# Kernel optimization log

Measured on AMD Instinct MI355X. Metric: run time of the kernel, lower is better.

## Reference

```python
import jax, jax.numpy as jnp
import numpy as np

T_STEPS = 64      # AR order p
MAX_T = 65536     # trajectory length
BATCH = 256       # number of sampled trajectories
STD = 0.3


def setup_inputs() -> dict:
    key = jax.random.key(0)
    k1, k2, k3 = jax.random.split(key, 3)
    raw = jax.random.normal(k1, (T_STEPS,), dtype=jnp.float32)
    # torch init: params / sum(|params|)
    params = raw / jnp.sum(jnp.abs(raw))
    bias = jax.random.uniform(k2, (1,), dtype=jnp.float32)
    noise = jax.random.normal(k3, (BATCH, MAX_T), dtype=jnp.float32)
    return {"params": params, "bias": bias, "noise": noise}


def _ar_means(params, bias, length):
    """AR(p) recurrence: mean_i = sum_k params[k] * x[i-1-k] + bias, x init = 0.
    State holds the last p values, most-recent-first (matches the reversed
    indexing inputs[i-1 : i-p-1 : -1] in the torch code)."""
    p = params.shape[0]

    def step(state, _):
        new = jnp.dot(state, params) + bias[0]
        state = jnp.concatenate([new[None], state[:-1]])
        return state, new

    init = jnp.zeros((p,), dtype=params.dtype)
    _, means = jax.lax.scan(step, init, None, length=length)
    return means  # [length]


def reference(params, bias, noise):
    # means of the Normal over the trajectory (deterministic, shared by batch)
    means = _ar_means(params, bias, noise.shape[1])  # [T]
    # reparameterized sample: actions = mean + std * eps, eps ~ N(0, 1)
    actions = means[None, :] + jnp.asarray(STD, noise.dtype) * noise  # [B, T]
    return actions
```

## Files before the change

### kernel.cpp

```cpp
#include <hip/hip_runtime.h>

#define T_LEN   65536
#define P       64
#define BASE    4096
#define K1_THREADS 256
#define W_TILE  1024
#define BCHUNK  8
#define VOFF    65536

typedef float f4 __attribute__((ext_vector_type(4)));


__constant__ unsigned char  TL_DST[14] = {2, 3,4, 6,5,8, 7,10,12,9, 14,11,13, 15};
__constant__ unsigned char  TL_SRC[14] = {1, 2,2, 3,4,4, 6,5,6,8, 7,10,12, 14};
__constant__ unsigned char  TL_DBL[14] = {1, 0,1, 1,0,1, 0,1,1,0, 1,0,0, 0};
__constant__ unsigned short TL_W[14]   = {192, 256,128, 192,256,64, 256,192,128,256, 192,256,256, 256};
__constant__ unsigned char  TL_OFF[7]  = {0,1,3,6,10,13,14};

__device__ __forceinline__ void tapV_wave(const float* __restrict__ td, int wd,
                                          const float* __restrict__ p,
                                          float* __restrict__ Vdst, int lane) {
    const int j = lane;
    float w0 = 0.f, w1 = 0.f, w2 = 0.f, w3 = 0.f;
    #pragma unroll
    for (int mm = 0; mm < 16; ++mm) w0 = fmaf(p[mm + j],      td[wd - 1  - mm], w0);
    #pragma unroll
    for (int mm = 0; mm < 16; ++mm) w1 = fmaf(p[16 + mm + j], td[wd - 17 - mm], w1);
    #pragma unroll
    for (int mm = 0; mm < 16; ++mm) w2 = fmaf(p[32 + mm + j], td[wd - 33 - mm], w2);
    #pragma unroll
    for (int mm = 0; mm < 16; ++mm) w3 = fmaf(p[48 + mm + j], td[wd - 49 - mm], w3);
    const float wj  = ((w0 + w1) + w2) + w3;
    const float wm1 = __shfl_up(wj, 1);
    Vdst[j] = (j == 0) ? wj : (wj - wm1);
    if (j == 63) Vdst[64] = 0.0f - wj;
}

__global__ __launch_bounds__(K1_THREADS, 1) void ar_k1(const float* __restrict__ params,
                                                       float* __restrict__ R) {
    __shared__ __align__(16) float Rl[BASE];
    __shared__ float p[128];
    __shared__ __align__(16) float Vs[68];
    __shared__ __align__(16) float Vnode[16][68];
    __shared__ __align__(16) float Tn[8][256];
    __shared__ __align__(16) float Tw[4][256];
    const int tid = threadIdx.x;
    if (tid < 128) p[tid] = (tid < P) ? params[tid] : 0.f;
    __syncthreads();

    if (tid < 64) {
        float z = 0.f;
        const float pk = p[tid];
        #pragma unroll 1
        for (int t = 0; t < 64; ++t) {
            float y  = __shfl(z, 0) + 1.0f;
            float zn = __shfl_down(z, 1);
            if (tid == 63) zn = 0.f;
            z = fmaf(pk, y, zn);
            if (tid == 0) Rl[t] = y;
        }
    }
    __syncthreads();

    #pragma unroll 1
    for (int L = 64; L <= BASE / 2; L <<= 1) {
        if (tid < 64) tapV_wave(Rl, L, p, Vs, tid);
        __syncthreads();
        if (tid < P) {
            const int tau = tid;
            float acc = Rl[tau];
            #pragma unroll
            for (int i = 0; i < P; ++i) {
                const int idx = (tau - i) > 0 ? (tau - i) : 0;
                const float v = (i <= tau) ? Vs[i] : 0.f;
                acc = fmaf(v, Rl[idx], acc);
            }
            Rl[L + tau] = acc;
        }
        {
            const f4* __restrict__ Rl4 = reinterpret_cast<const f4*>(Rl);
            f4* __restrict__ Rl4w = reinterpret_cast<f4*>(Rl);
            const f4* __restrict__ V4 = reinterpret_cast<const f4*>(Vs);
            const int nq = (L - 64) >> 2;
            #pragma unroll 1
            for (int q = tid; q < nq; q += K1_THREADS) {
                f4 w4[17];
                #pragma unroll
                for (int j = 0; j < 17; ++j) w4[j] = Rl4[q + j];
                float a0 = w4[16].x, a1 = w4[16].y, a2 = w4[16].z, a3 = w4[16].w;
                #pragma unroll
                for (int g = 0; g < 16; ++g) {
                    const f4 v  = V4[g];
                    const f4 hi = w4[16 - g];
                    const f4 lo = w4[15 - g];
                    a0 = fmaf(v.x, hi.x, a0); a1 = fmaf(v.x, hi.y, a1);
                    a2 = fmaf(v.x, hi.z, a2); a3 = fmaf(v.x, hi.w, a3);
                    a0 = fmaf(v.y, lo.w, a0); a1 = fmaf(v.y, hi.x, a1);
                    a2 = fmaf(v.y, hi.y, a2); a3 = fmaf(v.y, hi.z, a3);
                    a0 = fmaf(v.z, lo.z, a0); a1 = fmaf(v.z, lo.w, a1);
                    a2 = fmaf(v.z, hi.x, a2); a3 = fmaf(v.z, hi.y, a3);
                    a0 = fmaf(v.w, lo.y, a0); a1 = fmaf(v.w, lo.z, a1);
                    a2 = fmaf(v.w, lo.w, a2); a3 = fmaf(v.w, hi.x, a3);
                }
                const float v64 = Vs[64];
                a0 = fmaf(v64, w4[0].x, a0); a1 = fmaf(v64, w4[0].y, a1);
                a2 = fmaf(v64, w4[0].z, a2); a3 = fmaf(v64, w4[0].w, a3);
                f4 o; o.x = a0; o.y = a1; o.z = a2; o.w = a3;
                Rl4w[((L + 64) >> 2) + q] = o;
            }
        }
        __syncthreads();
    }

    #pragma unroll 1
    for (int j4 = tid; j4 < BASE / 4; j4 += K1_THREADS)
        reinterpret_cast<f4*>(R)[j4] = reinterpret_cast<const f4*>(Rl)[j4];

    if (tid < 64) tapV_wave(Rl + 3840, 256, p, Vnode[1], tid);
    __syncthreads();

    #pragma unroll 1
    for (int lvl = 0; lvl < 6; ++lvl) {
        const int w = tid >> 6, lane = tid & 63;
        const int n0 = TL_OFF[lvl], n1 = TL_OFF[lvl + 1];
        const int e = n0 + w;
        float* td = nullptr;
        int wd = 0;
        if (e < n1) {
            const int dst = TL_DST[e], src = TL_SRC[e];
            wd = TL_W[e];
            const float* __restrict__ Vsr = Vnode[src];
            const float* tail = (src == 1) ? (Rl + 3840) : Tn[src];
            const float* s0 = TL_DBL[e] ? (tail + 64) : (Rl + 3840);
            td = (dst <= 7) ? Tn[dst] : Tw[w];
            #pragma unroll 1
            for (int x = lane; x < wd; x += 64) {
                float acc = s0[x];
                #pragma unroll
                for (int i = 0; i <= P; ++i)
                    acc = fmaf(Vsr[i], s0[x - i], acc);
                td[x] = acc;
            }
        }
        __syncthreads();
        if (e < n1) tapV_wave(td, wd, p, Vnode[TL_DST[e]], lane);
        __syncthreads();
    }

    #pragma unroll 1
    for (int j = tid; j < 15 * 80; j += K1_THREADS) {
        const int k = j / 80 + 1, i = j - (k - 1) * 80;
        if (i < 65) R[VOFF + k * 80 + i] = Vnode[k][i];
    }
}

__global__ __launch_bounds__(256) void ar_out_fused(const float* __restrict__ R,
                                                    const float* __restrict__ bias,
                                                    const float* __restrict__ noise,
                                                    float* __restrict__ out) {
    __shared__ __align__(16) float win[1088];
    __shared__ __align__(16) float Vl[68];
    const int tid  = threadIdx.x;
    const int tile = blockIdx.x & 63;
    const int bc   = blockIdx.x >> 6;
    const int t0   = tile * W_TILE;
    const float b  = bias[0];
    const int k    = t0 >> 12;
    const f4* __restrict__ Rg4 = reinterpret_cast<const f4*>(R);

    f4 rt;
    if (k == 0) {
        const f4 r = Rg4[(t0 >> 2) + tid];
        rt.x = b * r.x; rt.y = b * r.y; rt.z = b * r.z; rt.w = b * r.w;
    } else {
        const int tau0 = t0 & 4095;
        if (tid < 65) Vl[tid] = R[VOFF + k * 80 + tid];
        f4* __restrict__ win4 = reinterpret_cast<f4*>(win);
        for (int j4 = tid; j4 < 272; j4 += 256) {
            const int u = tau0 - 64 + 4 * j4;
            f4 v;
            if (u >= 0) v = Rg4[u >> 2];
            else { v.x = 0.f; v.y = 0.f; v.z = 0.f; v.w = 0.f; }
            win4[j4] = v;
        }
        __syncthreads();
        const f4* __restrict__ V4 = reinterpret_cast<const f4*>(Vl);
        f4 w4[17];
        #pragma unroll
        for (int j = 0; j < 17; ++j) w4[j] = win4[tid + j];
        float a0 = w4[16].x, a1 = w4[16].y, a2 = w4[16].z, a3 = w4[16].w;
        #pragma unroll
        for (int g = 0; g < 16; ++g) {
            const f4 v  = V4[g];
            const f4 hi = w4[16 - g];
            const f4 lo = w4[15 - g];
            a0 = fmaf(v.x, hi.x, a0); a1 = fmaf(v.x, hi.y, a1);
            a2 = fmaf(v.x, hi.z, a2); a3 = fmaf(v.x, hi.w, a3);
            a0 = fmaf(v.y, lo.w, a0); a1 = fmaf(v.y, hi.x, a1);
            a2 = fmaf(v.y, hi.y, a2); a3 = fmaf(v.y, hi.z, a3);
            a0 = fmaf(v.z, lo.z, a0); a1 = fmaf(v.z, lo.w, a1);
            a2 = fmaf(v.z, hi.x, a2); a3 = fmaf(v.z, hi.y, a3);
            a0 = fmaf(v.w, lo.y, a0); a1 = fmaf(v.w, lo.z, a1);
            a2 = fmaf(v.w, lo.w, a2); a3 = fmaf(v.w, hi.x, a3);
        }
        const float v64 = Vl[64];
        a0 = fmaf(v64, w4[0].x, a0); a1 = fmaf(v64, w4[0].y, a1);
        a2 = fmaf(v64, w4[0].z, a2); a3 = fmaf(v64, w4[0].w, a3);
        rt.x = b * a0; rt.y = b * a1; rt.z = b * a2; rt.w = b * a3;
    }

    const int nb4 = T_LEN >> 2;
    const int col = (t0 >> 2) + tid;
    const f4* __restrict__ n4 = reinterpret_cast<const f4*>(noise);
    f4* __restrict__ o4 = reinterpret_cast<f4*>(out);
    #pragma unroll
    for (int bi = 0; bi < BCHUNK; ++bi) {
        const int idx = (bc * BCHUNK + bi) * nb4 + col;
        const f4 n = __builtin_nontemporal_load(n4 + idx);
        f4 o;
        o.x = fmaf(0.3f, n.x, rt.x);
        o.y = fmaf(0.3f, n.y, rt.y);
        o.z = fmaf(0.3f, n.z, rt.z);
        o.w = fmaf(0.3f, n.w, rt.w);
        __builtin_nontemporal_store(o, o4 + idx);
    }
}

extern "C" void kernel_launch(void* const* d_in, const int* in_sizes, int n_in,
                              void* d_out, int out_size, void* d_ws, size_t ws_size,
                              hipStream_t stream) {
    const float* params = (const float*)d_in[0];
    const float* bias   = (const float*)d_in[1];
    const float* noise  = (const float*)d_in[2];
    float* out = (float*)d_out;
    float* R   = (float*)d_ws;

    hipLaunchKernelGGL(ar_k1, dim3(1), dim3(K1_THREADS), 0, stream, params, R);
    hipLaunchKernelGGL(ar_out_fused, dim3(64 * 32), dim3(256), 0, stream,
                       R, bias, noise, out);
}
```

Baseline: 162.3 us.

## Restructure tap-vector tree into fixed four-level schedule with vectorized convolution

Replaces the table-driven six-level loop that builds the per-block tap vectors with a hard-coded four-level tree, where each wave extends a longer prefix buffer so fewer synchronized levels are needed. The scalar 65-tap convolution is replaced by a float4 register-tiled routine that loads a sliding window into registers and computes four outputs per lane. This aims to cut barrier count and LDS traffic in the serial single-block setup kernel. In exchange some waves do wider convolutions, and shared buffers grow.

Measured after the change: 162.5 us. No clear change (+0.1%).

```diff
diff --git a/kernel.cpp b/kernel.cpp
--- a/kernel.cpp
+++ b/kernel.cpp
@@ -11,12 +11,6 @@
 typedef float f4 __attribute__((ext_vector_type(4)));
 
 
-__constant__ unsigned char  TL_DST[14] = {2, 3,4, 6,5,8, 7,10,12,9, 14,11,13, 15};
-__constant__ unsigned char  TL_SRC[14] = {1, 2,2, 3,4,4, 6,5,6,8, 7,10,12, 14};
-__constant__ unsigned char  TL_DBL[14] = {1, 0,1, 1,0,1, 0,1,1,0, 1,0,0, 0};
-__constant__ unsigned short TL_W[14]   = {192, 256,128, 192,256,64, 256,192,128,256, 192,256,256, 256};
-__constant__ unsigned char  TL_OFF[7]  = {0,1,3,6,10,13,14};
-
 __device__ __forceinline__ void tapV_wave(const float* __restrict__ td, int wd,
                                           const float* __restrict__ p,
                                           float* __restrict__ Vdst, int lane) {
@@ -34,6 +28,42 @@
     const float wm1 = __shfl_up(wj, 1);
     Vdst[j] = (j == 0) ? wj : (wj - wm1);
     if (j == 63) Vdst[64] = 0.0f - wj;
+}
+
+__device__ __forceinline__ void treeconv(const float* __restrict__ tail,
+                                         int w_out,
+                                         const float* __restrict__ V,
+                                         float* __restrict__ outb, int lane) {
+    const f4* __restrict__ t4 = reinterpret_cast<const f4*>(tail);
+    const f4* __restrict__ V4 = reinterpret_cast<const f4*>(V);
+    f4* __restrict__ o4 = reinterpret_cast<f4*>(outb);
+    const int nq = w_out >> 2;
+    #pragma unroll 1
+    for (int q = lane; q < nq; q += 64) {
+        f4 w4[17];
+        #pragma unroll
+        for (int j = 0; j < 17; ++j) w4[j] = t4[q + j];
+        float a0 = w4[16].x, a1 = w4[16].y, a2 = w4[16].z, a3 = w4[16].w;
+        #pragma unroll
+        for (int g = 0; g < 16; ++g) {
+            const f4 v  = V4[g];
+            const f4 hi = w4[16 - g];
+            const f4 lo = w4[15 - g];
+            a0 = fmaf(v.x, hi.x, a0); a1 = fmaf(v.x, hi.y, a1);
+            a2 = fmaf(v.x, hi.z, a2); a3 = fmaf(v.x, hi.w, a3);
+            a0 = fmaf(v.y, lo.w, a0); a1 = fmaf(v.y, hi.x, a1);
+            a2 = fmaf(v.y, hi.y, a2); a3 = fmaf(v.y, hi.z, a3);
+            a0 = fmaf(v.z, lo.z, a0); a1 = fmaf(v.z, lo.w, a1);
+            a2 = fmaf(v.z, hi.x, a2); a3 = fmaf(v.z, hi.y, a3);
+            a0 = fmaf(v.w, lo.y, a0); a1 = fmaf(v.w, lo.z, a1);
+            a2 = fmaf(v.w, lo.w, a2); a3 = fmaf(v.w, hi.x, a3);
+        }
+        const float v64 = V[64];
+        a0 = fmaf(v64, w4[0].x, a0); a1 = fmaf(v64, w4[0].y, a1);
+        a2 = fmaf(v64, w4[0].z, a2); a3 = fmaf(v64, w4[0].w, a3);
+        f4 o; o.x = a0; o.y = a1; o.z = a2; o.w = a3;
+        o4[q] = o;
+    }
 }
 
 __global__ __launch_bounds__(K1_THREADS, 1) void ar_k1(const float* __restrict__ params,
@@ -42,8 +72,10 @@
     __shared__ float p[128];
     __shared__ __align__(16) float Vs[68];
     __shared__ __align__(16) float Vnode[16][68];
-    __shared__ __align__(16) float Tn[8][256];
-    __shared__ __align__(16) float Tw[4][256];
+    __shared__ __align__(16) float T2[448];
+    __shared__ __align__(16) float T4[384];
+    __shared__ __align__(16) float T8[320];
+    __shared__ __align__(16) float Tw[4][384];
     const int tid = threadIdx.x;
     if (tid < 128) p[tid] = (tid < P) ? params[tid] : 0.f;
     __syncthreads();
@@ -116,36 +148,38 @@
     for (int j4 = tid; j4 < BASE / 4; j4 += K1_THREADS)
         reinterpret_cast<f4*>(R)[j4] = reinterpret_cast<const f4*>(Rl)[j4];
 
-    if (tid < 64) tapV_wave(Rl + 3840, 256, p, Vnode[1], tid);
-    __syncthreads();
-
-    #pragma unroll 1
-    for (int lvl = 0; lvl < 6; ++lvl) {
-        const int w = tid >> 6, lane = tid & 63;
-        const int n0 = TL_OFF[lvl], n1 = TL_OFF[lvl + 1];
-        const int e = n0 + w;
-        float* td = nullptr;
-        int wd = 0;
-        if (e < n1) {
-            const int dst = TL_DST[e], src = TL_SRC[e];
-            wd = TL_W[e];
-            const float* __restrict__ Vsr = Vnode[src];
-            const float* tail = (src == 1) ? (Rl + 3840) : Tn[src];
-            const float* s0 = TL_DBL[e] ? (tail + 64) : (Rl + 3840);
-            td = (dst <= 7) ? Tn[dst] : Tw[w];
-            #pragma unroll 1
-            for (int x = lane; x < wd; x += 64) {
-                float acc = s0[x];
-                #pragma unroll
-                for (int i = 0; i <= P; ++i)
-                    acc = fmaf(Vsr[i], s0[x - i], acc);
-                td[x] = acc;
-            }
-        }
-        __syncthreads();
-        if (e < n1) tapV_wave(td, wd, p, Vnode[TL_DST[e]], lane);
-        __syncthreads();
-    }
+    const int w = tid >> 6, lane = tid & 63;
+    if (w == 0) {
+        tapV_wave(Rl + 3840, 256, p, Vnode[1], lane);
+        treeconv(Rl + 3584, 448, Vnode[1], T2, lane);
+        tapV_wave(T2, 448, p, Vnode[2], lane);
+    }
+    __syncthreads();
+    if (w == 0) {
+        treeconv(T2, 384, Vnode[2], T4, lane);
+        tapV_wave(T4, 384, p, Vnode[4], lane);
+    } else if (w == 1) {
+        treeconv(T2, 384, Vnode[1], Tw[1], lane);
+        tapV_wave(Tw[1], 384, p, Vnode[3], lane);
+    }
+    __syncthreads();
+    if (w == 0) {
+        treeconv(T4, 320, Vnode[4], T8, lane);
+        tapV_wave(T8, 320, p, Vnode[8], lane);
+    } else {
+        treeconv(T4, 320, Vnode[w], Tw[w], lane);
+        tapV_wave(Tw[w], 320, p, Vnode[4 + w], lane);
+    }
+    __syncthreads();
+    {
+        treeconv(T8, 256, Vnode[1 + w], Tw[w], lane);
+        tapV_wave(Tw[w], 256, p, Vnode[9 + w], lane);
+        if (w < 3) {
+            treeconv(T8, 256, Vnode[5 + w], Tw[w], lane);
+            tapV_wave(Tw[w], 256, p, Vnode[13 + w], lane);
+        }
+    }
+    __syncthreads();
 
     #pragma unroll 1
     for (int j = tid; j < 15 * 80; j += K1_THREADS) {
```
